# Kernel tuning notes

Measured on AMD Instinct MI355X. Metric: run time of the kernel, lower is better.

## Reference

```python
import jax, jax.numpy as jnp
import numpy as np

H = 16  # num_heads


def setup_inputs() -> dict:
    key = jax.random.key(0)
    ks = jax.random.split(key, 7)
    S, HID, D = 8192, 1280, 80
    n_chunks = 8
    x = jax.random.normal(ks[0], (S, HID), dtype=jnp.float32)
    cos = jax.random.uniform(ks[1], (S, D), dtype=jnp.float32)
    sin = jax.random.uniform(ks[2], (S, D), dtype=jnp.float32)
    Wqkv = jax.random.normal(ks[3], (HID, 3 * HID), dtype=jnp.float32) * (HID ** -0.5)
    bqkv = jnp.zeros((3 * HID,), dtype=jnp.float32)
    Wproj = jax.random.normal(ks[4], (HID, HID), dtype=jnp.float32) * (HID ** -0.5)
    bproj = jnp.zeros((HID,), dtype=jnp.float32)
    cu_seqlens = (jnp.arange(n_chunks + 1, dtype=jnp.int32) * (S // n_chunks))
    return {"x": x, "cos": cos, "sin": sin, "Wqkv": Wqkv, "bqkv": bqkv,
            "Wproj": Wproj, "bproj": bproj, "cu_seqlens": cu_seqlens}


def _apply_rotary(t, cos, sin):
    # t: (S, H, D); cos/sin: (S, D)
    d2 = t.shape[-1] // 2
    x1, x2 = t[..., :d2], t[..., d2:]
    rotated = jnp.concatenate([-x2, x1], axis=-1)
    return t * cos[:, None, :] + rotated * sin[:, None, :]


def reference(x, cos, sin, Wqkv, bqkv, Wproj, bproj, cu_seqlens):
    S, HID = x.shape
    D = HID // H
    inv_scale = 1.0 / np.sqrt(D)
    qkv = (x @ Wqkv + bqkv).reshape(S, 3, H, D)
    q, k, v = qkv[:, 0], qkv[:, 1], qkv[:, 2]  # each (S, H, D)
    q = _apply_rotary(q, cos, sin)
    k = _apply_rotary(k, cos, sin)
    # Equal-size windows: reshape to (n_chunks, L, H, D) -> block-diagonal attention.
    C = cu_seqlens.shape[0] - 1
    L = S // C
    qc = q.reshape(C, L, H, D)
    kc = k.reshape(C, L, H, D)
    vc = v.reshape(C, L, H, D)
    scores = jnp.einsum('cihd,cjhd->chij', qc, kc) * inv_scale
    probs = jax.nn.softmax(scores.astype(jnp.float32), axis=-1).astype(x.dtype)
    out = jnp.einsum('chij,cjhd->cihd', probs, vc)  # (C, L, H, D)
    out = out.reshape(S, HID)
    return out @ Wproj + bproj
```

## Files before the change

### kernel.cpp

```cpp
#include <hip/hip_runtime.h>
#include <math.h>
#include <stdint.h>

#define S_LEN 8192
#define HID   1280
#define NH    16
#define HD    80
#define LCH   1024
#define NCH   8

typedef __attribute__((ext_vector_type(8))) short bf16x8;
typedef __attribute__((ext_vector_type(4))) float f32x4;

__device__ __forceinline__ uint16_t f2bf(float f) {
    union { float f; uint32_t u; } v; v.f = f;
    uint32_t r = v.u + 0x7FFF + ((v.u >> 16) & 1);
    return (uint16_t)(r >> 16);
}
__device__ __forceinline__ float bf2f(uint16_t h) {
    union { uint32_t u; float f; } v; v.u = ((uint32_t)h) << 16;
    return v.f;
}
__device__ __forceinline__ uint32_t pk2(float a, float b) {
    union { float f; uint32_t u; } x, y; x.f = a; y.f = b;
    return (x.u >> 16) | (y.u & 0xFFFF0000u);
}

__device__ __forceinline__ void glds16(const void* g, void* l) {
    __builtin_amdgcn_global_load_lds(
        (const __attribute__((address_space(1))) uint32_t*)g,
        (__attribute__((address_space(3))) uint32_t*)l,
        16, 0, 0);
}

#define MFMA16(a, b, c) __builtin_amdgcn_mfma_f32_16x16x32_bf16(a, b, c, 0, 0, 0)
#define SB()  __builtin_amdgcn_sched_barrier(0)
#define BAR() __builtin_amdgcn_s_barrier()

template<int N> __device__ __forceinline__ void vmwait() {
    if constexpr (N == 0) asm volatile("s_waitcnt vmcnt(0)" ::: "memory");
    else if constexpr (N == 3) asm volatile("s_waitcnt vmcnt(3)" ::: "memory");
    else if constexpr (N == 4) asm volatile("s_waitcnt vmcnt(4)" ::: "memory");
}

__device__ __forceinline__ void stage_tile(const char* gsrc, char* dst, int w,
                                           int kt, int nbytes)
{
    const char* sp = gsrc + (size_t)kt * 64;
    int off = w * 1024;
    glds16(sp + (size_t)off * 40, dst + off);
    off += 8192;
    if (off < nbytes) glds16(sp + (size_t)off * 40, dst + off);
}

__global__ __launch_bounds__(256)
void xsplit_kernel(const float* __restrict__ x, uint16_t* __restrict__ xh,
                   uint16_t* __restrict__ xl)
{
    int idx = (blockIdx.x * 256 + threadIdx.x) * 4;
    float4 v = *(const float4*)(x + idx);
    ushort4 hi, lo;
    hi.x = f2bf(v.x); lo.x = f2bf(v.x - bf2f(hi.x));
    hi.y = f2bf(v.y); lo.y = f2bf(v.y - bf2f(hi.y));
    hi.z = f2bf(v.z); lo.z = f2bf(v.z - bf2f(hi.z));
    hi.w = f2bf(v.w); lo.w = f2bf(v.w - bf2f(hi.w));
    *(ushort4*)(xh + idx) = hi;
    *(ushort4*)(xl + idx) = lo;
}

template<int ND>
__global__ __launch_bounds__(256)
void wsplit_kernel(const float* __restrict__ W, uint16_t* __restrict__ Wth,
                   uint16_t* __restrict__ Wtl)
{
    __shared__ float t[32][33];
    const int tid = threadIdx.x;
    const int n0 = blockIdx.x * 32;
    const int k0 = blockIdx.y * 32;
    for (int i = tid; i < 1024; i += 256) {
        int r = i >> 5, c = i & 31;
        t[r][c] = W[(size_t)(k0 + r) * ND + n0 + c];
    }
    __syncthreads();
    for (int i = tid; i < 1024; i += 256) {
        int r = i >> 5, c = i & 31;
        float f = t[c][r];
        uint16_t hi = f2bf(f);
        size_t o = (size_t)(n0 + r) * HID + k0 + c;
        Wth[o] = hi;
        Wtl[o] = f2bf(f - bf2f(hi));
    }
}

template<int ND, int BN, int NWN, int EPI, int W1>
__global__ __launch_bounds__(512, 2)
void gemm8p(const uint16_t* __restrict__ Ahp, const uint16_t* __restrict__ Alp,
            const uint16_t* __restrict__ Bth, const uint16_t* __restrict__ Btl,
            const float* __restrict__ bias, float* __restrict__ oF,
            uint16_t* __restrict__ oq, uint16_t* __restrict__ ok,
            uint16_t* __restrict__ ov)
{
    constexpr int NWM = 8 / NWN;
    constexpr int MI  = 256 / (NWM * 16);
    constexpr int NI  = BN / (NWN * 16);
    constexpr int ABYTES = 256 * 64;
    constexpr int BBYTES = BN * 64;
    constexpr int NT = HID / 32;
    static_assert(BN % (NWN * 16) == 0, "tile split");

    __shared__ __align__(1024) uint16_t AsH[2][ABYTES / 2];
    __shared__ __align__(1024) uint16_t AsL[2][ABYTES / 2];
    __shared__ __align__(1024) uint16_t BsH[2][BBYTES / 2];
    __shared__ __align__(1024) uint16_t BsL[2][BBYTES / 2];

    const int tid  = threadIdx.x;
    const int w    = tid >> 6;
    const int lane = tid & 63;
    const int quad = lane >> 4;
    const int l16  = lane & 15;
    const int wm   = w / NWN;
    const int wn   = w % NWN;

    const int n0 = blockIdx.x * BN;
    const int m0 = blockIdx.y * 256;

    const size_t stg = (size_t)(lane >> 2) * (HID * 2)
                     + (size_t)(((lane & 3) ^ ((lane >> 3) & 3)) << 4);
    const char* gAh = (const char*)Ahp + (size_t)m0 * (HID * 2) + stg;
    const char* gAl = (const char*)Alp + (size_t)m0 * (HID * 2) + stg;
    const char* gBh = (const char*)Bth + (size_t)n0 * (HID * 2) + stg;
    const char* gBl = (const char*)Btl + (size_t)n0 * (HID * 2) + stg;

    const int swz  = (quad ^ ((l16 >> 1) & 3)) << 4;
    const int aoff = (wm * (MI * 16) + l16) * 64 + swz;
    const int boff = (wn * (NI * 16) + l16) * 64 + swz;

    f32x4 acc[MI][NI];
    #pragma unroll
    for (int mi = 0; mi < MI; ++mi)
        #pragma unroll
        for (int ni = 0; ni < NI; ++ni) acc[mi][ni] = (f32x4){0.f, 0.f, 0.f, 0.f};

    stage_tile(gAh, (char*)AsH[0], w, 0, ABYTES);
    stage_tile(gBh, (char*)BsH[0], w, 0, BBYTES);
    stage_tile(gBl, (char*)BsL[0], w, 0, BBYTES);
    stage_tile(gAl, (char*)AsL[0], w, 0, ABYTES);
    SB(); vmwait<W1>(); BAR(); SB();

    for (int kt = 0; kt < NT - 1; ++kt) {
        const int s = kt & 1, t = s ^ 1;
        bf16x8 ah[MI], bh[NI];

        #pragma unroll
        for (int mi = 0; mi < MI; ++mi)
            ah[mi] = *(const bf16x8*)((const char*)AsH[s] + aoff + mi * 1024);
        #pragma unroll
        for (int ni = 0; ni < NI; ++ni)
            bh[ni] = *(const bf16x8*)((const char*)BsH[s] + boff + ni * 1024);
        stage_tile(gAh, (char*)AsH[t], w, kt + 1, ABYTES);
        stage_tile(gBh, (char*)BsH[t], w, kt + 1, BBYTES);
        SB(); vmwait<W1>(); BAR(); SB();
        __builtin_amdgcn_s_setprio(1);
        #pragma unroll
        for (int mi = 0; mi < MI; ++mi)
            #pragma unroll
            for (int ni = 0; ni < NI; ++ni)
                acc[mi][ni] = MFMA16(ah[mi], bh[ni], acc[mi][ni]);
        __builtin_amdgcn_s_setprio(0);

        bf16x8 bl[NI];
        #pragma unroll
        for (int ni = 0; ni < NI; ++ni)
            bl[ni] = *(const bf16x8*)((const char*)BsL[s] + boff + ni * 1024);
        stage_tile(gBl, (char*)BsL[t], w, kt + 1, BBYTES);
        stage_tile(gAl, (char*)AsL[t], w, kt + 1, ABYTES);
        SB(); BAR(); SB();
        __builtin_amdgcn_s_setprio(1);
        #pragma unroll
        for (int mi = 0; mi < MI; ++mi)
            #pragma unroll
            for (int ni = 0; ni < NI; ++ni)
                acc[mi][ni] = MFMA16(ah[mi], bl[ni], acc[mi][ni]);
        __builtin_amdgcn_s_setprio(0);

        bf16x8 al[MI];
        #pragma unroll
        for (int mi = 0; mi < MI; ++mi)
            al[mi] = *(const bf16x8*)((const char*)AsL[s] + aoff + mi * 1024);
        SB(); vmwait<W1>(); BAR(); SB();
        __builtin_amdgcn_s_setprio(1);
        #pragma unroll
        for (int mi = 0; mi < MI; ++mi)
            #pragma unroll
            for (int ni = 0; ni < NI; ++ni)
                acc[mi][ni] = MFMA16(al[mi], bh[ni], acc[mi][ni]);
        __builtin_amdgcn_s_setprio(0);
    }

    {
        const int s = (NT - 1) & 1;
        bf16x8 ah[MI], bh[NI];
        #pragma unroll
        for (int mi = 0; mi < MI; ++mi)
            ah[mi] = *(const bf16x8*)((const char*)AsH[s] + aoff + mi * 1024);
        #pragma unroll
        for (int ni = 0; ni < NI; ++ni)
            bh[ni] = *(const bf16x8*)((const char*)BsH[s] + boff + ni * 1024);
        SB(); vmwait<0>(); BAR(); SB();
        __builtin_amdgcn_s_setprio(1);
        #pragma unroll
        for (int mi = 0; mi < MI; ++mi)
            #pragma unroll
            for (int ni = 0; ni < NI; ++ni)
                acc[mi][ni] = MFMA16(ah[mi], bh[ni], acc[mi][ni]);
        __builtin_amdgcn_s_setprio(0);

        bf16x8 bl[NI];
        #pragma unroll
        for (int ni = 0; ni < NI; ++ni)
            bl[ni] = *(const bf16x8*)((const char*)BsL[s] + boff + ni * 1024);
        #pragma unroll
        for (int mi = 0; mi < MI; ++mi)
            #pragma unroll
            for (int ni = 0; ni < NI; ++ni)
                acc[mi][ni] = MFMA16(ah[mi], bl[ni], acc[mi][ni]);

        bf16x8 al[MI];
        #pragma unroll
        for (int mi = 0; mi < MI; ++mi)
            al[mi] = *(const bf16x8*)((const char*)AsL[s] + aoff + mi * 1024);
        #pragma unroll
        for (int mi = 0; mi < MI; ++mi)
            #pragma unroll
            for (int ni = 0; ni < NI; ++ni)
                acc[mi][ni] = MFMA16(al[mi], bh[ni], acc[mi][ni]);
    }

    #pragma unroll
    for (int ni = 0; ni < NI; ++ni) {
        const int n = n0 + wn * (NI * 16) + ni * 16 + l16;
        const float bv = bias[n];
        if constexpr (EPI) {
            const int tq  = n / HID;
            const int rem = n - tq * HID;
            const int h   = rem / HD;
            const int d   = rem - h * HD;
            #pragma unroll
            for (int mi = 0; mi < MI; ++mi) {
                const int mb = m0 + wm * (MI * 16) + mi * 16 + quad * 4;
                if (tq == 2) {
                    ushort4 pv;
                    pv.x = f2bf(acc[mi][ni][0] + bv);
                    pv.y = f2bf(acc[mi][ni][1] + bv);
                    pv.z = f2bf(acc[mi][ni][2] + bv);
                    pv.w = f2bf(acc[mi][ni][3] + bv);
                    *(ushort4*)&ov[((size_t)h * HD + d) * S_LEN + mb] = pv;
                } else {
                    uint16_t* dst = (tq == 0) ? oq : ok;
                    #pragma unroll
                    for (int r = 0; r < 4; ++r)
                        dst[((size_t)h * S_LEN + (mb + r)) * HD + d] =
                            f2bf(acc[mi][ni][r] + bv);
                }
            }
        } else {
            #pragma unroll
            for (int mi = 0; mi < MI; ++mi) {
                const int mb = m0 + wm * (MI * 16) + mi * 16 + quad * 4;
                #pragma unroll
                for (int r = 0; r < 4; ++r)
                    oF[(size_t)(mb + r) * ND + n] = acc[mi][ni][r] + bv;
            }
        }
    }
}

__global__ __launch_bounds__(256)
void rope_kernel(uint16_t* __restrict__ qb, uint16_t* __restrict__ kb,
                 const float* __restrict__ cosb, const float* __restrict__ sinb)
{
    int idx = blockIdx.x * 256 + threadIdx.x;
    int d = idx % 40;
    int t = idx / 40;
    int s = t % S_LEN;
    int h = t / S_LEN;
    size_t base = ((size_t)h * S_LEN + s) * HD;
    float c1 = cosb[s * HD + d],      s1 = sinb[s * HD + d];
    float c2 = cosb[s * HD + d + 40], s2 = sinb[s * HD + d + 40];
    float q1 = bf2f(qb[base + d]), q2 = bf2f(qb[base + d + 40]);
    qb[base + d]      = f2bf(q1 * c1 - q2 * s1);
    qb[base + d + 40] = f2bf(q2 * c2 + q1 * s2);
    float k1 = bf2f(kb[base + d]), k2 = bf2f(kb[base + d + 40]);
    kb[base + d]      = f2bf(k1 * c1 - k2 * s1);
    kb[base + d + 40] = f2bf(k2 * c2 + k1 * s2);
}

#define BQ 256
#define BK 64

__device__ __forceinline__ void kstage(const char* kg, char* dst, int w, int lane)
{
    int p = w * 1024 + lane * 16;
    {
        int row = p >> 7;
        int sl  = (p >> 4) & 7;
        glds16(kg + row * 160 + ((sl ^ (row & 7)) << 4), dst + p);
    }
    int p2 = p + 8192;
    if (p2 < 10240) {
        int q   = p2 - 8192;
        int row = q >> 5;
        int sl  = (q >> 4) & 1;
        glds16(kg + row * 160 + 128 + (sl << 4), dst + p2);
    }
}

__global__ __launch_bounds__(512, 4)
void attn_kernel(const uint16_t* __restrict__ qb, const uint16_t* __restrict__ kb,
                 const uint16_t* __restrict__ vt,
                 uint16_t* __restrict__ abh, uint16_t* __restrict__ abl)
{
    __shared__ __align__(16) uint16_t smemA[BQ * HD];
    __shared__ __align__(16) uint16_t ksm[2][BK * HD];
    __shared__ __align__(16) uint16_t vsm[HD * BK];

    const int tid  = threadIdx.x;
    const int w    = tid >> 6;
    const int lane = tid & 63;
    const int quad = lane >> 4;
    const int l16  = lane & 15;

    const int qt = blockIdx.x;
    const int h  = blockIdx.y;
    const int c  = blockIdx.z;
    const int q0 = c * LCH + qt * BQ;

    uint16_t (*psw)[68] = (uint16_t(*)[68])smemA + w * 32;

    {
        const char* qg = (const char*)(qb + ((size_t)h * S_LEN + q0) * HD);
        for (int off = w * 1024; off < BQ * HD * 2; off += 8192)
            glds16(qg + off + lane * 16, (char*)smemA + off);
    }
    __syncthreads();

    bf16x8 qfr[2][3];
    #pragma unroll
    for (int mi = 0; mi < 2; ++mi) {
        const int row = w * 32 + mi * 16 + l16;
        qfr[mi][0] = *(const bf16x8*)&smemA[row * HD + quad * 8];
        qfr[mi][1] = *(const bf16x8*)&smemA[row * HD + 32 + quad * 8];
        bf16x8 z = {0, 0, 0, 0, 0, 0, 0, 0};
        qfr[mi][2] = (quad < 2) ? *(const bf16x8*)&smemA[row * HD + 64 + quad * 8] : z;
    }

    bf16x8 vf5;
    {
        short o = (l16 == 0) ? (short)0x3F80 : (short)0;
        vf5 = (bf16x8){o, o, o, o, o, o, o, o};
    }

    f32x4 Oacc[2][6];
    #pragma unroll
    for (int mi = 0; mi < 2; ++mi)
        #pragma unroll
        for (int d = 0; d < 6; d++) Oacc[mi][d] = (f32x4){0.f, 0.f, 0.f, 0.f};

    const float C2 = 0.11180339887498949f * 1.4426950408889634f;
    const char* kg0 = (const char*)(kb + ((size_t)h * S_LEN + c * LCH) * HD);
    const size_t vrow_stride = (size_t)S_LEN * 2;
    const char* vg0 = (const char*)vt + (size_t)h * HD * S_LEN * 2 + (size_t)(c * LCH) * 2;

    kstage(kg0, (char*)&ksm[0][0], w, lane);

    for (int kt = 0; kt < LCH / BK; ++kt) {
        __syncthreads();

        {
            const char* vg = vg0 + (size_t)(kt * BK) * 2;
            for (int off = w * 1024; off < HD * BK * 2; off += 8192) {
                int o   = off + lane * 16;
                int row = o >> 7;
                int col = o & 127;
                glds16(vg + (size_t)row * vrow_stride + (col ^ ((row & 7) << 4)),
                       (char*)vsm + off);
            }
        }

        const char* ksb = (const char*)&ksm[kt & 1][0];
        #pragma unroll
        for (int ns = 0; ns < 4; ++ns) {
            const int kr = ns * 16 + l16;
            const int sw = (kr & 7) << 4;
            bf16x8 kf0 = *(const bf16x8*)(ksb + kr * 128 + ((quad * 16) ^ sw));
            bf16x8 kf1 = *(const bf16x8*)(ksb + kr * 128 + ((64 + quad * 16) ^ sw));
            bf16x8 z = {0, 0, 0, 0, 0, 0, 0, 0};
            bf16x8 kf2 = (quad < 2)
                ? *(const bf16x8*)(ksb + 8192 + kr * 32 + quad * 16) : z;
            #pragma unroll
            for (int mi = 0; mi < 2; ++mi) {
                f32x4 s = (f32x4){0.f, 0.f, 0.f, 0.f};
                s = MFMA16(kf0, qfr[mi][0], s);
                s = MFMA16(kf1, qfr[mi][1], s);
                s = MFMA16(kf2, qfr[mi][2], s);
                float e0 = exp2f(s[0] * C2);
                float e1 = exp2f(s[1] * C2);
                float e2 = exp2f(s[2] * C2);
                float e3 = exp2f(s[3] * C2);
                *(uint2*)&psw[mi * 16 + l16][ns * 16 + quad * 4] =
                    (uint2){pk2(e0, e1), pk2(e2, e3)};
            }
        }

        __syncthreads();

        if (kt + 1 < LCH / BK)
            kstage(kg0 + (size_t)(kt + 1) * BK * HD * 2,
                   (char*)&ksm[(kt + 1) & 1][0], w, lane);

        #pragma unroll
        for (int kc = 0; kc < 2; ++kc) {
            bf16x8 pf[2];
            #pragma unroll
            for (int mi = 0; mi < 2; ++mi) {
                const uint16_t* pp = &psw[mi * 16 + l16][kc * 32 + quad * 8];
                ((uint2*)&pf[mi])[0] = *(const uint2*)(pp);
                ((uint2*)&pf[mi])[1] = *(const uint2*)(pp + 4);
            }
            #pragma unroll
            for (int ds = 0; ds < 5; ++ds) {
                const int vr = ds * 16 + l16;
                bf16x8 vf = *(const bf16x8*)((const char*)vsm + vr * 128 +
                    ((kc * 64 + quad * 16) ^ ((vr & 7) << 4)));
                #pragma unroll
                for (int mi = 0; mi < 2; ++mi)
                    Oacc[mi][ds] = MFMA16(pf[mi], vf, Oacc[mi][ds]);
            }
            #pragma unroll
            for (int mi = 0; mi < 2; ++mi)
                Oacc[mi][5] = MFMA16(pf[mi], vf5, Oacc[mi][5]);
        }
    }

    #pragma unroll
    for (int mi = 0; mi < 2; ++mi)
        #pragma unroll
        for (int r = 0; r < 4; ++r) {
            float l = __shfl(Oacc[mi][5][r], lane & 48);
            float inv = 1.f / l;
            const int srow = q0 + w * 32 + mi * 16 + quad * 4 + r;
            const size_t rowbase = (size_t)srow * HID + h * HD;
            #pragma unroll
            for (int ds = 0; ds < 5; ++ds) {
                float f = Oacc[mi][ds][r] * inv;
                uint16_t hi = f2bf(f);
                abh[rowbase + ds * 16 + l16] = hi;
                abl[rowbase + ds * 16 + l16] = f2bf(f - bf2f(hi));
            }
        }
}

extern "C" void kernel_launch(void* const* d_in, const int* in_sizes, int n_in,
                              void* d_out, int out_size, void* d_ws, size_t ws_size,
                              hipStream_t stream)
{
    const float* x     = (const float*)d_in[0];
    const float* cosb  = (const float*)d_in[1];
    const float* sinb  = (const float*)d_in[2];
    const float* Wqkv  = (const float*)d_in[3];
    const float* bqkv  = (const float*)d_in[4];
    const float* Wproj = (const float*)d_in[5];
    const float* bproj = (const float*)d_in[6];
    float* out = (float*)d_out;

    const size_t E = (size_t)NH * S_LEN * HD;
    uint16_t* qb  = (uint16_t*)d_ws;
    uint16_t* kb  = qb + E;
    uint16_t* vt  = kb + E;
    uint16_t* xh  = vt + E;
    uint16_t* xl  = xh + E;
    uint16_t* wth = xl + E;
    uint16_t* wtl = wth + (size_t)3 * HID * HID;

    xsplit_kernel<<<(S_LEN * HID) / (256 * 4), 256, 0, stream>>>(x, xh, xl);
    wsplit_kernel<3 * HID><<<dim3(3 * HID / 32, HID / 32), 256, 0, stream>>>(Wqkv, wth, wtl);
    gemm8p<3 * HID, 256, 4, 1, 4>
        <<<dim3(3 * HID / 256, S_LEN / 256), 512, 0, stream>>>(
        xh, xl, wth, wtl, bqkv, nullptr, qb, kb, vt);
    rope_kernel<<<(S_LEN * NH * 40) / 256, 256, 0, stream>>>(qb, kb, cosb, sinb);
    attn_kernel<<<dim3(LCH / BQ, NH, NCH), 512, 0, stream>>>(qb, kb, vt, xh, xl);
    wsplit_kernel<HID><<<dim3(HID / 32, HID / 32), 256, 0, stream>>>(Wproj, wth, wtl);
    gemm8p<HID, 160, 2, 0, 3>
        <<<dim3(HID / 160, S_LEN / 256), 512, 0, stream>>>(
        xh, xl, wth, wtl, bproj, out, nullptr, nullptr, nullptr);
}
```

Before: 479.7 us.

## Simplify GEMM pipeline to one barrier per k-step, add XCD swizzle, vectorize RoPE

Result: slower. 565.3 us (+17.8%).

```diff
diff --git a/kernel.cpp b/kernel.cpp
--- a/kernel.cpp
+++ b/kernel.cpp
@@ -10,6 +10,7 @@
 #define NCH   8
 
 typedef __attribute__((ext_vector_type(8))) short bf16x8;
+typedef __attribute__((ext_vector_type(8))) unsigned short u16x8;
 typedef __attribute__((ext_vector_type(4))) float f32x4;
 
 __device__ __forceinline__ uint16_t f2bf(float f) {
@@ -37,10 +38,8 @@
 #define SB()  __builtin_amdgcn_sched_barrier(0)
 #define BAR() __builtin_amdgcn_s_barrier()
 
-template<int N> __device__ __forceinline__ void vmwait() {
-    if constexpr (N == 0) asm volatile("s_waitcnt vmcnt(0)" ::: "memory");
-    else if constexpr (N == 3) asm volatile("s_waitcnt vmcnt(3)" ::: "memory");
-    else if constexpr (N == 4) asm volatile("s_waitcnt vmcnt(4)" ::: "memory");
+__device__ __forceinline__ void vmwait0() {
+    asm volatile("s_waitcnt vmcnt(0)" ::: "memory");
 }
 
 __device__ __forceinline__ void stage_tile(const char* gsrc, char* dst, int w,
@@ -92,9 +91,9 @@
     }
 }
 
-template<int ND, int BN, int NWN, int EPI, int W1>
+template<int ND, int BN, int NWN, int EPI>
 __global__ __launch_bounds__(512, 2)
-void gemm8p(const uint16_t* __restrict__ Ahp, const uint16_t* __restrict__ Alp,
+void gemm1b(const uint16_t* __restrict__ Ahp, const uint16_t* __restrict__ Alp,
             const uint16_t* __restrict__ Bth, const uint16_t* __restrict__ Btl,
             const float* __restrict__ bias, float* __restrict__ oF,
             uint16_t* __restrict__ oq, uint16_t* __restrict__ ok,
@@ -106,7 +105,11 @@
     constexpr int ABYTES = 256 * 64;
     constexpr int BBYTES = BN * 64;
     constexpr int NT = HID / 32;
+    constexpr int NBX = ND / BN;
+    constexpr int NWG = NBX * 32;
+    constexpr int CPX = NWG / 8;
     static_assert(BN % (NWN * 16) == 0, "tile split");
+    static_assert(NWG % 8 == 0, "xcd swizzle");
 
     __shared__ __align__(1024) uint16_t AsH[2][ABYTES / 2];
     __shared__ __align__(1024) uint16_t AsL[2][ABYTES / 2];
@@ -121,8 +124,10 @@
     const int wm   = w / NWN;
     const int wn   = w % NWN;
 
-    const int n0 = blockIdx.x * BN;
-    const int m0 = blockIdx.y * 256;
+    const int hwid = blockIdx.y * NBX + blockIdx.x;
+    const int nid  = (hwid & 7) * CPX + (hwid >> 3);
+    const int n0 = (nid >> 5) * BN;
+    const int m0 = (nid & 31) * 256;
 
     const size_t stg = (size_t)(lane >> 2) * (HID * 2)
                      + (size_t)(((lane & 3) ^ ((lane >> 3) & 3)) << 4);
@@ -145,95 +150,54 @@
     stage_tile(gBh, (char*)BsH[0], w, 0, BBYTES);
     stage_tile(gBl, (char*)BsL[0], w, 0, BBYTES);
     stage_tile(gAl, (char*)AsL[0], w, 0, ABYTES);
-    SB(); vmwait<W1>(); BAR(); SB();
-
-    for (int kt = 0; kt < NT - 1; ++kt) {
+
+    for (int kt = 0; kt < NT; ++kt) {
         const int s = kt & 1, t = s ^ 1;
+
+        SB(); vmwait0(); BAR(); SB();
+
+        if (kt + 1 < NT) {
+            stage_tile(gAh, (char*)AsH[t], w, kt + 1, ABYTES);
+            stage_tile(gBh, (char*)BsH[t], w, kt + 1, BBYTES);
+            stage_tile(gBl, (char*)BsL[t], w, kt + 1, BBYTES);
+            stage_tile(gAl, (char*)AsL[t], w, kt + 1, ABYTES);
+        }
+
         bf16x8 ah[MI], bh[NI];
-
         #pragma unroll
         for (int mi = 0; mi < MI; ++mi)
             ah[mi] = *(const bf16x8*)((const char*)AsH[s] + aoff + mi * 1024);
         #pragma unroll
         for (int ni = 0; ni < NI; ++ni)
             bh[ni] = *(const bf16x8*)((const char*)BsH[s] + boff + ni * 1024);
-        stage_tile(gAh, (char*)AsH[t], w, kt + 1, ABYTES);
-        stage_tile(gBh, (char*)BsH[t], w, kt + 1, BBYTES);
-        SB(); vmwait<W1>(); BAR(); SB();
+
         __builtin_amdgcn_s_setprio(1);
         #pragma unroll
         for (int mi = 0; mi < MI; ++mi)
             #pragma unroll
             for (int ni = 0; ni < NI; ++ni)
                 acc[mi][ni] = MFMA16(ah[mi], bh[ni], acc[mi][ni]);
-        __builtin_amdgcn_s_setprio(0);
 
         bf16x8 bl[NI];
         #pragma unroll
         for (int ni = 0; ni < NI; ++ni)
             bl[ni] = *(const bf16x8*)((const char*)BsL[s] + boff + ni * 1024);
-        stage_tile(gBl, (char*)BsL[t], w, kt + 1, BBYTES);
-        stage_tile(gAl, (char*)AsL[t], w, kt + 1, ABYTES);
-        SB(); BAR(); SB();
-        __builtin_amdgcn_s_setprio(1);
         #pragma unroll
         for (int mi = 0; mi < MI; ++mi)
             #pragma unroll
             for (int ni = 0; ni < NI; ++ni)
                 acc[mi][ni] = MFMA16(ah[mi], bl[ni], acc[mi][ni]);
-        __builtin_amdgcn_s_setprio(0);
 
         bf16x8 al[MI];
         #pragma unroll
         for (int mi = 0; mi < MI; ++mi)
             al[mi] = *(const bf16x8*)((const char*)AsL[s] + aoff + mi * 1024);
-        SB(); vmwait<W1>(); BAR(); SB();
-        __builtin_amdgcn_s_setprio(1);
         #pragma unroll
         for (int mi = 0; mi < MI; ++mi)
             #pragma unroll
             for (int ni = 0; ni < NI; ++ni)
                 acc[mi][ni] = MFMA16(al[mi], bh[ni], acc[mi][ni]);
         __builtin_amdgcn_s_setprio(0);
-    }
-
-    {
-        const int s = (NT - 1) & 1;
-        bf16x8 ah[MI], bh[NI];
-        #pragma unroll
-        for (int mi = 0; mi < MI; ++mi)
-            ah[mi] = *(const bf16x8*)((const char*)AsH[s] + aoff + mi * 1024);
-        #pragma unroll
-        for (int ni = 0; ni < NI; ++ni)
-            bh[ni] = *(const bf16x8*)((const char*)BsH[s] + boff + ni * 1024);
-        SB(); vmwait<0>(); BAR(); SB();
-        __builtin_amdgcn_s_setprio(1);
-        #pragma unroll
-        for (int mi = 0; mi < MI; ++mi)
-            #pragma unroll
-            for (int ni = 0; ni < NI; ++ni)
-                acc[mi][ni] = MFMA16(ah[mi], bh[ni], acc[mi][ni]);
-        __builtin_amdgcn_s_setprio(0);
-
-        bf16x8 bl[NI];
-        #pragma unroll
-        for (int ni = 0; ni < NI; ++ni)
-            bl[ni] = *(const bf16x8*)((const char*)BsL[s] + boff + ni * 1024);
-        #pragma unroll
-        for (int mi = 0; mi < MI; ++mi)
-            #pragma unroll
-            for (int ni = 0; ni < NI; ++ni)
-                acc[mi][ni] = MFMA16(ah[mi], bl[ni], acc[mi][ni]);
-
-        bf16x8 al[MI];
-        #pragma unroll
-        for (int mi = 0; mi < MI; ++mi)
-            al[mi] = *(const bf16x8*)((const char*)AsL[s] + aoff + mi * 1024);
-        #pragma unroll
-        for (int mi = 0; mi < MI; ++mi)
-            #pragma unroll
-            for (int ni = 0; ni < NI; ++ni)
-                acc[mi][ni] = MFMA16(al[mi], bh[ni], acc[mi][ni]);
     }
 
     #pragma unroll
@@ -279,20 +243,43 @@
 void rope_kernel(uint16_t* __restrict__ qb, uint16_t* __restrict__ kb,
                  const float* __restrict__ cosb, const float* __restrict__ sinb)
 {
-    int idx = blockIdx.x * 256 + threadIdx.x;
-    int d = idx % 40;
-    int t = idx / 40;
-    int s = t % S_LEN;
-    int h = t / S_LEN;
-    size_t base = ((size_t)h * S_LEN + s) * HD;
-    float c1 = cosb[s * HD + d],      s1 = sinb[s * HD + d];
-    float c2 = cosb[s * HD + d + 40], s2 = sinb[s * HD + d + 40];
-    float q1 = bf2f(qb[base + d]), q2 = bf2f(qb[base + d + 40]);
-    qb[base + d]      = f2bf(q1 * c1 - q2 * s1);
-    qb[base + d + 40] = f2bf(q2 * c2 + q1 * s2);
-    float k1 = bf2f(kb[base + d]), k2 = bf2f(kb[base + d + 40]);
-    kb[base + d]      = f2bf(k1 * c1 - k2 * s1);
-    kb[base + d + 40] = f2bf(k2 * c2 + k1 * s2);
+    const int t = blockIdx.x * 256 + threadIdx.x;
+    const int s = t & (S_LEN - 1);
+    uint16_t* qr = qb + (size_t)t * HD;
+    uint16_t* kr = kb + (size_t)t * HD;
+    const float* cr = cosb + (size_t)s * HD;
+    const float* sr = sinb + (size_t)s * HD;
+    #pragma unroll
+    for (int ch = 0; ch < 5; ++ch) {
+        const int d = ch * 8;
+        u16x8 q1 = *(const u16x8*)(qr + d);
+        u16x8 q2 = *(const u16x8*)(qr + d + 40);
+        u16x8 k1 = *(const u16x8*)(kr + d);
+        u16x8 k2 = *(const u16x8*)(kr + d + 40);
+        float c1[8], c2[8], s1[8], s2[8];
+        *(float4*)&c1[0] = *(const float4*)(cr + d);
+        *(float4*)&c1[4] = *(const float4*)(cr + d + 4);
+        *(float4*)&c2[0] = *(const float4*)(cr + d + 40);
+        *(float4*)&c2[4] = *(const float4*)(cr + d + 44);
+        *(float4*)&s1[0] = *(const float4*)(sr + d);
+        *(float4*)&s1[4] = *(const float4*)(sr + d + 4);
+        *(float4*)&s2[0] = *(const float4*)(sr + d + 40);
+        *(float4*)&s2[4] = *(const float4*)(sr + d + 44);
+        u16x8 o1, o2, p1, p2;
+        #pragma unroll
+        for (int j = 0; j < 8; ++j) {
+            float q1f = bf2f((uint16_t)q1[j]), q2f = bf2f((uint16_t)q2[j]);
+            o1[j] = f2bf(q1f * c1[j] - q2f * s1[j]);
+            o2[j] = f2bf(q2f * c2[j] + q1f * s2[j]);
+            float k1f = bf2f((uint16_t)k1[j]), k2f = bf2f((uint16_t)k2[j]);
+            p1[j] = f2bf(k1f * c1[j] - k2f * s1[j]);
+            p2[j] = f2bf(k2f * c2[j] + k1f * s2[j]);
+        }
+        *(u16x8*)(qr + d)      = o1;
+        *(u16x8*)(qr + d + 40) = o2;
+        *(u16x8*)(kr + d)      = p1;
+        *(u16x8*)(kr + d + 40) = p2;
+    }
 }
 
 #define BQ 256
@@ -484,13 +471,13 @@
 
     xsplit_kernel<<<(S_LEN * HID) / (256 * 4), 256, 0, stream>>>(x, xh, xl);
     wsplit_kernel<3 * HID><<<dim3(3 * HID / 32, HID / 32), 256, 0, stream>>>(Wqkv, wth, wtl);
-    gemm8p<3 * HID, 256, 4, 1, 4>
+    gemm1b<3 * HID, 256, 4, 1>
         <<<dim3(3 * HID / 256, S_LEN / 256), 512, 0, stream>>>(
         xh, xl, wth, wtl, bqkv, nullptr, qb, kb, vt);
-    rope_kernel<<<(S_LEN * NH * 40) / 256, 256, 0, stream>>>(qb, kb, cosb, sinb);
+    rope_kernel<<<(NH * S_LEN) / 256, 256, 0, stream>>>(qb, kb, cosb, sinb);
     attn_kernel<<<dim3(LCH / BQ, NH, NCH), 512, 0, stream>>>(qb, kb, vt, xh, xl);
     wsplit_kernel<HID><<<dim3(HID / 32, HID / 32), 256, 0, stream>>>(Wproj, wth, wtl);
-    gemm8p<HID, 160, 2, 0, 3>
+    gemm1b<HID, 160, 2, 0>
         <<<dim3(HID / 160, S_LEN / 256), 512, 0, stream>>>(
         xh, xl, wth, wtl, bproj, out, nullptr, nullptr, nullptr);
 }
```
